# Kernel tuning notes

Measured on AMD Instinct MI355X. Metric: run time of the kernel, lower is better.

The kernel has to match this reference:

```python
import jax, jax.numpy as jnp
import numpy as np

H = 516      # LSTM hidden per direction
T = 512      # encoder source length
B = 64       # batch
NY = 20      # decoder target length
SEQ = 20     # seqLen == decoder input feature == n classes


def _u(key, shape, k):
    return jax.random.uniform(key, shape, jnp.float32, -k, k)


def setup_inputs() -> dict:
    key = jax.random.key(0)
    ks = jax.random.split(key, 26)
    kh = float(1.0 / np.sqrt(H))
    ka = float(1.0 / np.sqrt(2 * H * 2))
    inp = {}
    inp['x'] = jax.random.normal(ks[0], (T, B, 4), jnp.float32)
    inp['y'] = jax.random.normal(ks[1], (NY, B, SEQ), jnp.float32)
    inp['label'] = jax.random.randint(ks[2], (NY, B), 0, SEQ)
    inp['expand_W'] = _u(ks[3], (256, 4), 0.5)
    inp['expand_b'] = _u(ks[4], (256,), 0.5)
    # encoder biLSTM: 2 layers x 2 directions; PyTorch gate order i,f,g,o
    inp['eWi0'] = _u(ks[5], (2, 4 * H, 256), kh)
    inp['eWh0'] = _u(ks[6], (2, 4 * H, H), kh)
    inp['eb0'] = _u(ks[7], (2, 4 * H), kh)
    inp['eWi1'] = _u(ks[8], (2, 4 * H, 2 * H), kh)
    inp['eWh1'] = _u(ks[9], (2, 4 * H, H), kh)
    inp['eb1'] = _u(ks[10], (2, 4 * H), kh)
    # decoder biLSTM
    inp['dWi0'] = _u(ks[11], (2, 4 * H, SEQ), kh)
    inp['dWh0'] = _u(ks[12], (2, 4 * H, H), kh)
    inp['db0'] = _u(ks[13], (2, 4 * H), kh)
    inp['dWi1'] = _u(ks[14], (2, 4 * H, 2 * H), kh)
    inp['dWh1'] = _u(ks[15], (2, 4 * H, H), kh)
    inp['db1'] = _u(ks[16], (2, 4 * H), kh)
    # concat attention: Linear(2064, 1032) + v
    inp['attn_W'] = _u(ks[17], (2 * H, 4 * H), ka)
    inp['attn_b'] = _u(ks[18], (2 * H,), ka)
    inp['attn_v'] = _u(ks[19], (2 * H,), ka)
    inp['concat_W'] = _u(ks[20], (2 * H, 4 * H), ka)
    inp['concat_b'] = _u(ks[21], (2 * H,), ka)
    inp['out_W'] = _u(ks[22], (SEQ, 2 * H), float(1.0 / np.sqrt(2 * H)))
    inp['out_b'] = _u(ks[23], (SEQ,), float(1.0 / np.sqrt(2 * H)))
    return inp


def _cell(x, h, c, Wi, Wh, b):
    g = x @ Wi.T + h @ Wh.T + b
    i, f, gg, o = jnp.split(g, 4, axis=-1)
    c2 = jax.nn.sigmoid(f) * c + jax.nn.sigmoid(i) * jnp.tanh(gg)
    h2 = jax.nn.sigmoid(o) * jnp.tanh(c2)
    return h2, c2


def _run_dir(xs, h0, c0, Wi, Wh, b, reverse):
    def step(carry, xt):
        h, c = _cell(xt, carry[0], carry[1], Wi, Wh, b)
        return (h, c), h
    (hT, cT), ys = jax.lax.scan(step, (h0, c0), xs, reverse=reverse)
    return ys, hT, cT


def _bilstm(xs, Wi0, Wh0, b0, Wi1, Wh1, b1):
    z = jnp.zeros((xs.shape[1], H), xs.dtype)
    out = xs
    hs, cs = [], []
    for Wi, Wh, b in ((Wi0, Wh0, b0), (Wi1, Wh1, b1)):
        yf, hf, cf = _run_dir(out, z, z, Wi[0], Wh[0], b[0], False)
        yb, hb, cb = _run_dir(out, z, z, Wi[1], Wh[1], b[1], True)
        out = jnp.concatenate([yf, yb], -1)
        hs += [hf, hb]
        cs += [cf, cb]
    return out, jnp.stack(hs), jnp.stack(cs)


def reference(x, y, label, expand_W, expand_b, eWi0, eWh0, eb0, eWi1, eWh1, eb1,
              dWi0, dWh0, db0, dWi1, dWh1, db1, attn_W, attn_b, attn_v,
              concat_W, concat_b, out_W, out_b):
    xe = x @ expand_W.T + expand_b                       # [T,B,256]
    outenc, h0, c0 = _bilstm(xe, eWi0, eWh0, eb0, eWi1, eWh1, eb1)  # [T,B,1032],[4,B,H]
    lab = label.astype(jnp.int32)

    def dec_step(carry, inp):
        h, c, loss = carry
        yi, li = inp                                    # [B,SEQ], [B]
        # 1-step bidirectional 2-layer decoder LSTM (seq len 1 => fwd==bwd path)
        h0f, c0f = _cell(yi, h[0], c[0], dWi0[0], dWh0[0], db0[0])
        h0b, c0b = _cell(yi, h[1], c[1], dWi0[1], dWh0[1], db0[1])
        l0 = jnp.concatenate([h0f, h0b], -1)
        h1f, c1f = _cell(l0, h[2], c[2], dWi1[0], dWh1[0], db1[0])
        h1b, c1b = _cell(l0, h[3], c[3], dWi1[1], dWh1[1], db1[1])
        outdec = jnp.concatenate([h1f, h1b], -1)        # [B,1032]
        # concat attention over encoder outputs
        hid = jnp.broadcast_to(outdec[None], outenc.shape)
        energy = jnp.tanh(jnp.concatenate([hid, outenc], -1) @ attn_W.T + attn_b)
        score = jnp.einsum('h,tbh->tb', attn_v, energy)
        aw = jax.nn.softmax(score, axis=0)              # softmax over src_len
        context = jnp.einsum('tb,tbh->bh', aw, outenc)
        co = jnp.tanh(jnp.concatenate([outdec, context], -1) @ concat_W.T + concat_b)
        logits = co @ out_W.T + out_b                   # [B,SEQ]
        ls = jax.nn.log_softmax(logits, -1)
        ce = -jnp.take_along_axis(ls, li[:, None], 1).mean()
        h_new = jnp.stack([h0f, h0b, h1f, h1b])
        c_new = jnp.stack([c0f, c0b, c1f, c1b])
        return (h_new, c_new, loss + ce), None

    init = (h0, c0, jnp.float32(0.0))
    (_, _, loss), _ = jax.lax.scan(dec_step, init, (y, lab))
    return loss
```

## Files before the change

kernel.cpp:

```cpp
#include <hip/hip_runtime.h>
#include <hip/hip_bf16.h>
#include <cstdint>

typedef __attribute__((ext_vector_type(8))) short s8v;
typedef __attribute__((ext_vector_type(4))) float f4v;

#define DEV __device__ __forceinline__

constexpr int Hh  = 516;
constexpr int HP  = 544;
constexpr int FH  = 2064;
constexpr int NP  = 2176;
constexpr int TT  = 512;
constexpr int BB  = 64;
constexpr int LD2 = 1088;
constexpr int LDE = 1152;
constexpr int CS  = 528;
constexpr int XR  = 584;

DEV float bf2f(unsigned short u){ return __builtin_bit_cast(float, (unsigned)u<<16); }
DEV unsigned short f2bf(float f){
  unsigned u = __builtin_bit_cast(unsigned, f);
  u += 0x7fffu + ((u>>16)&1u);
  return (unsigned short)(u>>16);
}
DEV float sigf(float x){ return 1.f/(1.f+__expf(-x)); }
DEV float tanhfast(float x){ float e=__expf(2.f*x); return 1.f - 2.f/(e+1.f); }

DEV __attribute__((always_inline))
unsigned long long aload(const unsigned long long* p){
  return __hip_atomic_load(p, __ATOMIC_RELAXED, __HIP_MEMORY_SCOPE_AGENT);
}

DEV void cell_x1(f4v (&acc)[4],
                 const unsigned short* __restrict__ X1, int ld1,
                 const unsigned short* __restrict__ W1, int ldw1, int K1,
                 int j0)
{
  const int tid = threadIdx.x;
  const int w = tid>>6, lane = tid&63, p = lane&15, q = lane>>4;
  const unsigned short* wrow = W1 + (size_t)(w*HP + j0 + p)*ldw1 + q*8;
  for (int kk = 0; kk < (K1>>5); ++kk) {
    s8v bfr = *(const s8v*)(wrow + (size_t)kk*32);
    #pragma unroll
    for (int m = 0; m < 4; ++m) {
      s8v afr = *(const s8v*)(X1 + (size_t)(m*16+p)*ld1 + kk*32 + q*8);
      acc[m] = __builtin_amdgcn_mfma_f32_16x16x32_bf16(afr, bfr, acc[m], 0, 0, 0);
    }
  }
}

template<bool BYP>
DEV void cell_rest(f4v (&acc)[4],
                   const unsigned short* __restrict__ X2g,
                   const unsigned short* __restrict__ W2,
                   const float* __restrict__ bias,
                   float* __restrict__ cst,
                   unsigned* __restrict__ hout,
                   unsigned short* __restrict__ yout, int ldy, int ycol,
                   int j0)
{
  __shared__ __align__(16) unsigned short Xs[64*XR];
  __shared__ float gbuf[4][64][17];
  const int tid = threadIdx.x;
  const int w = tid>>6, lane = tid&63, p = lane&15, q = lane>>4;

  {
    int row = tid >> 2, c4 = (tid & 3) * 4;
    unsigned long long tmp[34];
    #pragma unroll
    for (int it = 0; it < 34; ++it) {
      const unsigned long long* s =
        (const unsigned long long*)(X2g + (size_t)row*HP + it*16 + c4);
      tmp[it] = BYP ? aload(s) : *s;
    }
    #pragma unroll
    for (int it = 0; it < 34; ++it)
      *(unsigned long long*)(Xs + row*XR + it*16 + c4) = tmp[it];
  }
  __syncthreads();

  {
    const unsigned short* wrow = W2 + (size_t)(w*HP + j0 + p)*HP + q*8;
    #pragma unroll
    for (int kk = 0; kk < HP/32; ++kk) {
      s8v bfr = *(const s8v*)(wrow + kk*32);
      #pragma unroll
      for (int m = 0; m < 4; ++m) {
        s8v afr = *(const s8v*)(Xs + (m*16+p)*XR + kk*32 + q*8);
        acc[m] = __builtin_amdgcn_mfma_f32_16x16x32_bf16(afr, bfr, acc[m], 0, 0, 0);
      }
    }
  }
  {
    int j = j0 + p;
    float bval = (j < Hh) ? bias[w*Hh + j] : 0.f;
    #pragma unroll
    for (int m = 0; m < 4; ++m)
      #pragma unroll
      for (int r = 0; r < 4; ++r)
        gbuf[w][m*16 + q*4 + r][p] = acc[m][r] + bval;
  }
  __syncthreads();
  {
    int b = tid & 63, j4 = tid >> 6;
    unsigned short hb[4];
    #pragma unroll
    for (int ii = 0; ii < 4; ++ii) {
      int jj = j4*4 + ii, jg = j0 + jj;
      float gi = gbuf[0][b][jj], gf = gbuf[1][b][jj];
      float gg = gbuf[2][b][jj], go = gbuf[3][b][jj];
      bool valid = jg < Hh;
      float c  = valid ? cst[(size_t)b*CS + jg] : 0.f;
      float c2 = sigf(gf)*c + sigf(gi)*tanhfast(gg);
      float h  = sigf(go)*tanhfast(c2);
      if (valid) cst[(size_t)b*CS + jg] = c2;
      hb[ii] = valid ? f2bf(h) : (unsigned short)0;
    }
    unsigned hu0 = (unsigned)hb[0] | ((unsigned)hb[1] << 16);
    unsigned hu1 = (unsigned)hb[2] | ((unsigned)hb[3] << 16);
    unsigned* hp = hout + (size_t)b*(HP/2) + (j0 + j4*4)/2;
    __hip_atomic_store(hp,   hu0, __ATOMIC_RELAXED, __HIP_MEMORY_SCOPE_AGENT);
    __hip_atomic_store(hp+1, hu1, __ATOMIC_RELAXED, __HIP_MEMORY_SCOPE_AGENT);
    unsigned long long yv = (unsigned long long)hu0 | ((unsigned long long)hu1 << 32);
    *(unsigned long long*)(yout + (size_t)b*ldy + ycol + j0 + j4*4) = yv;
  }
  __syncthreads();
}

__global__ void __launch_bounds__(256) enc_rnn(
  const unsigned short* __restrict__ Wi,
  int ldwi, int K1,
  const unsigned short* __restrict__ Xseq,
  int ld1,
  const unsigned short* __restrict__ Wh,
  const float* __restrict__ eb,
  unsigned short* __restrict__ yout,
  unsigned short* __restrict__ hbufs,
  float* __restrict__ cst,
  unsigned* flags)
{
  int d = blockIdx.x / 33, j0 = (blockIdx.x % 33) * 16;
  const unsigned short* W1 = Wi + (size_t)d*NP*ldwi;
  const unsigned short* W2 = Wh + (size_t)d*NP*HP;
  const float* bias = eb + (size_t)d*FH;
  float* cs = cst + (size_t)d*BB*CS;
  unsigned* flg = flags + (size_t)d*TT;
  for (int t = 0; t < TT; ++t) {
    int tf = d ? (TT-1-t) : t;
    const unsigned short* hin = hbufs + (size_t)((t&1)*2 + d)*BB*HP;
    unsigned* hout = (unsigned*)(hbufs + (size_t)(((t+1)&1)*2 + d)*BB*HP);
    f4v acc[4] = {};
    cell_x1(acc, Xseq + (size_t)tf*BB*ld1, ld1, W1, ldwi, K1, j0);
    if (t > 0 && threadIdx.x == 0) {
      while (__hip_atomic_load(flg + (t-1), __ATOMIC_RELAXED,
                               __HIP_MEMORY_SCOPE_AGENT) < 33u)
        __builtin_amdgcn_s_sleep(1);
    }
    __syncthreads();
    cell_rest<true>(acc, hin, W2, bias, cs, hout,
                    yout + (size_t)tf*BB*LD2, LD2, d*HP, j0);
    if (threadIdx.x == 0)
      __hip_atomic_fetch_add(flg + t, 1u, __ATOMIC_RELAXED, __HIP_MEMORY_SCOPE_AGENT);
  }
}

__global__ void __launch_bounds__(256) dec_cell(
  const unsigned short* __restrict__ X1, int ld1, int K1,
  const unsigned short* __restrict__ hin_base,
  unsigned short* __restrict__ hout_base,
  int loff,
  const unsigned short* __restrict__ Wi, int ldwi,
  const unsigned short* __restrict__ Whh,
  const float* __restrict__ dbias,
  float* __restrict__ cstates,
  unsigned short* __restrict__ yout, int ldy)
{
  int d = blockIdx.x / 33, j0 = (blockIdx.x % 33) * 16;
  f4v acc[4] = {};
  cell_x1(acc, X1, ld1, Wi + (size_t)d*NP*ldwi, ldwi, K1, j0);
  cell_rest<false>(acc,
    hin_base + (size_t)(loff+d)*BB*HP,
    Whh + (size_t)d*NP*HP,
    dbias + (size_t)d*FH,
    cstates + (size_t)(loff+d)*BB*CS,
    (unsigned*)(hout_base + (size_t)(loff+d)*BB*HP),
    yout, ldy, d*HP, j0);
}

__global__ void __launch_bounds__(256) gemm_bt(
  const unsigned short* __restrict__ A, int lda,
  const unsigned short* __restrict__ W, int ldw,
  unsigned short* __restrict__ C, int ldc, int K,
  const float* __restrict__ bias, int nbias)
{
  __shared__ __align__(16) unsigned short As[128*72];
  __shared__ __align__(16) unsigned short Ws[128*72];
  int tid = threadIdx.x, w = tid>>6, lane = tid&63, p = lane&15, q = lane>>4;
  int wm = w & 1, wn = w >> 1;
  size_t m0 = (size_t)blockIdx.x * 128;
  int n0 = blockIdx.y * 128;
  f4v acc[4][4] = {};
  for (int k0 = 0; k0 < K; k0 += 64) {
    __syncthreads();
    #pragma unroll
    for (int i = 0; i < 4; ++i) {
      int v = tid + i*256;
      int row = v >> 3, k8 = (v & 7) * 8;
      *(s8v*)(As + row*72 + k8) = *(const s8v*)(A + (m0+row)*lda + k0 + k8);
      *(s8v*)(Ws + row*72 + k8) = *(const s8v*)(W + (size_t)(n0+row)*ldw + k0 + k8);
    }
    __syncthreads();
    #pragma unroll
    for (int kk = 0; kk < 2; ++kk) {
      s8v af[4], bf[4];
      #pragma unroll
      for (int i = 0; i < 4; ++i) {
        af[i] = *(const s8v*)(As + (wm*64 + i*16 + p)*72 + kk*32 + q*8);
        bf[i] = *(const s8v*)(Ws + (wn*64 + i*16 + p)*72 + kk*32 + q*8);
      }
      #pragma unroll
      for (int mt = 0; mt < 4; ++mt)
        #pragma unroll
        for (int nt = 0; nt < 4; ++nt)
          acc[mt][nt] = __builtin_amdgcn_mfma_f32_16x16x32_bf16(af[mt], bf[nt], acc[mt][nt], 0,0,0);
    }
  }
  #pragma unroll
  for (int mt = 0; mt < 4; ++mt)
    #pragma unroll
    for (int nt = 0; nt < 4; ++nt)
      #pragma unroll
      for (int r = 0; r < 4; ++r) {
        size_t row = m0 + wm*64 + mt*16 + q*4 + r;
        int col = n0 + wn*64 + nt*16 + p;
        float v = acc[mt][nt][r];
        if (bias && col < nbias) v += bias[col];
        C[row*ldc + col] = f2bf(v);
      }
}

__global__ void __launch_bounds__(256) gemm64(
  const unsigned short* __restrict__ A, int lda,
  const unsigned short* __restrict__ W, int ldw, int K,
  const float* __restrict__ bias, int nbias, int mode,
  void* __restrict__ C, int ldc)
{
  int tid = threadIdx.x, w = tid>>6, lane = tid&63, p = lane&15, q = lane>>4;
  int n0 = blockIdx.x*64 + w*16;
  f4v acc[4] = {};
  const unsigned short* wrow = W + (size_t)(n0+p)*ldw + q*8;
  for (int kk = 0; kk < K/32; ++kk) {
    s8v bfr = *(const s8v*)(wrow + kk*32);
    #pragma unroll
    for (int m = 0; m < 4; ++m) {
      s8v afr = *(const s8v*)(A + (size_t)(m*16+p)*lda + kk*32 + q*8);
      acc[m] = __builtin_amdgcn_mfma_f32_16x16x32_bf16(afr, bfr, acc[m], 0,0,0);
    }
  }
  #pragma unroll
  for (int m = 0; m < 4; ++m)
    #pragma unroll
    for (int r = 0; r < 4; ++r) {
      int b = m*16 + q*4 + r, col = n0 + p;
      float v = acc[m][r];
      if (bias && col < nbias) v += bias[col];
      if (mode == 2) v = tanhfast(v);
      if (mode == 0) ((float*)C)[(size_t)b*ldc + col] = v;
      else ((unsigned short*)C)[(size_t)b*ldc + col] = f2bf(v);
    }
}

__global__ void __launch_bounds__(256) attn_score(
  const unsigned short* __restrict__ encp,
  const float* __restrict__ qv,
  const float* __restrict__ av,
  float* __restrict__ score)
{
  int t = blockIdx.x;
  int w = threadIdx.x>>6, lane = threadIdx.x&63;
  float vv[17];
  #pragma unroll
  for (int i = 0; i < 17; ++i) { int n = i*64+lane; vv[i] = (n < 1032) ? av[n] : 0.f; }
  const unsigned short* erow = encp + (size_t)t*BB*LDE;
  for (int bb = 0; bb < 16; ++bb) {
    int b = w*16 + bb;
    const unsigned short* e = erow + (size_t)b*LDE;
    const float* qb = qv + (size_t)b*LDE;
    float s = 0.f;
    #pragma unroll
    for (int i = 0; i < 17; ++i) {
      int n = i*64 + lane;
      s += vv[i] * tanhfast(bf2f(e[n]) + qb[n]);
    }
    #pragma unroll
    for (int off = 32; off; off >>= 1) s += __shfl_xor(s, off);
    if (lane == 0) score[(size_t)t*BB + b] = s;
  }
}

__global__ void __launch_bounds__(256) attn_ctx(
  const float* __restrict__ score,
  const unsigned short* __restrict__ outenc,
  unsigned short* __restrict__ Xc)
{
  __shared__ float aw[512];
  __shared__ float red[4];
  int tid = threadIdx.x, w = tid>>6, lane = tid&63;
  int b = blockIdx.x >> 1, half = blockIdx.x & 1;
  float s0 = score[(size_t)tid*BB + b];
  float s1 = score[(size_t)(tid+256)*BB + b];
  float m = fmaxf(s0, s1);
  #pragma unroll
  for (int off = 32; off; off >>= 1) m = fmaxf(m, __shfl_xor(m, off));
  if (lane == 0) red[w] = m;
  __syncthreads();
  m = fmaxf(fmaxf(red[0], red[1]), fmaxf(red[2], red[3]));
  __syncthreads();
  float e0 = __expf(s0 - m), e1 = __expf(s1 - m);
  aw[tid] = e0; aw[tid+256] = e1;
  float ss = e0 + e1;
  #pragma unroll
  for (int off = 32; off; off >>= 1) ss += __shfl_xor(ss, off);
  if (lane == 0) red[w] = ss;
  __syncthreads();
  float inv = 1.f / (red[0]+red[1]+red[2]+red[3]);
  float acc0 = 0.f, acc1 = 0.f, acc2 = 0.f;
  const unsigned short* base = outenc + (size_t)b*LD2 + half*HP;
  for (int t = 0; t < 512; ++t) {
    float a_ = aw[t];
    const unsigned short* orow = base + (size_t)t*BB*LD2;
    acc0 += a_ * bf2f(orow[tid]);
    acc1 += a_ * bf2f(orow[tid+256]);
    if (tid < 32) acc2 += a_ * bf2f(orow[tid+512]);
  }
  unsigned short* dst = Xc + (size_t)b*2176 + 1088 + half*HP;
  dst[tid]      = f2bf(acc0*inv);
  dst[tid+256]  = f2bf(acc1*inv);
  if (tid < 32) dst[tid+512] = f2bf(acc2*inv);
}

__global__ void ce_k(const float* __restrict__ logits,
                     const int* __restrict__ label,
                     float* __restrict__ out)
{
  int b = threadIdx.x;
  const float* lr = logits + (size_t)b*64;
  float m = -1e30f;
  for (int n = 0; n < 20; ++n) m = fmaxf(m, lr[n]);
  float s = 0.f;
  for (int n = 0; n < 20; ++n) s += __expf(lr[n] - m);
  int li = label[b];
  float ce = -(lr[li] - m - __logf(s));
  #pragma unroll
  for (int off = 32; off; off >>= 1) ce += __shfl_xor(ce, off);
  if (b == 0) atomicAdd(out, ce * (1.f/64.f));
}

__global__ void __launch_bounds__(256) expand_k(
  const float* __restrict__ x, const float* __restrict__ eW,
  const float* __restrict__ ebi, unsigned short* __restrict__ xe)
{
  int row = blockIdx.x, j = threadIdx.x;
  const float* xr = x + (size_t)row*4;
  float4 wv = ((const float4*)eW)[j];
  float v = ebi[j] + xr[0]*wv.x + xr[1]*wv.y + xr[2]*wv.z + xr[3]*wv.w;
  xe[(size_t)row*256 + j] = f2bf(v);
}

__global__ void __launch_bounds__(256) dec_init(
  const unsigned short* __restrict__ encH,
  const float* __restrict__ encC,
  unsigned short* __restrict__ decH,
  float* __restrict__ decC)
{
  int tid = blockIdx.x*256 + threadIdx.x;
  int nth = gridDim.x*256;
  for (int i = tid; i < 4*BB*HP; i += nth) {
    int k = i / (BB*HP), rem = i % (BB*HP);
    decH[i] = encH[((size_t)(k>>1)*4 + (k&1))*BB*HP + rem];
  }
  for (int i = tid; i < 4*BB*CS; i += nth) {
    int k = i / (BB*CS), rem = i % (BB*CS);
    decC[i] = encC[((size_t)(k>>1)*2 + (k&1))*BB*CS + rem];
  }
}

struct PackA {
  const float *eWi0,*eWh0,*eWi1,*eWh1,*dWi0,*dWh0,*dWi1,*dWh1,*aW,*cW,*oW,*y;
  unsigned short *pEWi0,*pEWh0,*pEWi1,*pEWh1,*pDWi0,*pDWh0,*pDWi1,*pDWh1,
                 *pAW1,*pAW2,*pCW,*pOW,*pY;
};

__global__ void __launch_bounds__(256) pack_k(PackA a){
  int job = blockIdx.y, row = blockIdx.x, tid = threadIdx.x;
  if (job < 16) {
    if (row >= NP) return;
    int d = job & 1, jt = job >> 1;
    int g = row / HP, jj = row % HP; bool vr = jj < Hh; int sr = g*Hh + jj;
    if (jt == 0) {
      unsigned short* dst = a.pEWi0 + ((size_t)d*NP + row)*256;
      const float* s = a.eWi0 + ((size_t)d*FH + sr)*256;
      for (int k = tid; k < 256; k += 256) dst[k] = vr ? f2bf(s[k]) : 0;
    } else if (jt == 1) {
      unsigned short* dst = a.pEWh0 + ((size_t)d*NP + row)*HP;
      const float* s = a.eWh0 + ((size_t)d*FH + sr)*Hh;
      for (int k = tid; k < HP; k += 256) dst[k] = (vr && k < Hh) ? f2bf(s[k]) : 0;
    } else if (jt == 2) {
      unsigned short* dst = a.pEWi1 + ((size_t)d*NP + row)*LD2;
      const float* s = a.eWi1 + ((size_t)d*FH + sr)*1032;
      for (int k = tid; k < LD2; k += 256) {
        int d2 = k/HP, j = k%HP;
        dst[k] = (vr && j < Hh) ? f2bf(s[d2*Hh + j]) : 0;
      }
    } else if (jt == 3) {
      unsigned short* dst = a.pEWh1 + ((size_t)d*NP + row)*HP;
      const float* s = a.eWh1 + ((size_t)d*FH + sr)*Hh;
      for (int k = tid; k < HP; k += 256) dst[k] = (vr && k < Hh) ? f2bf(s[k]) : 0;
    } else if (jt == 4) {
      unsigned short* dst = a.pDWi0 + ((size_t)d*NP + row)*64;
      const float* s = a.dWi0 + ((size_t)d*FH + sr)*20;
      for (int k = tid; k < 64; k += 256) dst[k] = (vr && k < 20) ? f2bf(s[k]) : 0;
    } else if (jt == 5) {
      unsigned short* dst = a.pDWh0 + ((size_t)d*NP + row)*HP;
      const float* s = a.dWh0 + ((size_t)d*FH + sr)*Hh;
      for (int k = tid; k < HP; k += 256) dst[k] = (vr && k < Hh) ? f2bf(s[k]) : 0;
    } else if (jt == 6) {
      unsigned short* dst = a.pDWi1 + ((size_t)d*NP + row)*LD2;
      const float* s = a.dWi1 + ((size_t)d*FH + sr)*1032;
      for (int k = tid; k < LD2; k += 256) {
        int d2 = k/HP, j = k%HP;
        dst[k] = (vr && j < Hh) ? f2bf(s[d2*Hh + j]) : 0;
      }
    } else {
      unsigned short* dst = a.pDWh1 + ((size_t)d*NP + row)*HP;
      const float* s = a.dWh1 + ((size_t)d*FH + sr)*Hh;
      for (int k = tid; k < HP; k += 256) dst[k] = (vr && k < Hh) ? f2bf(s[k]) : 0;
    }
  } else if (job == 16 || job == 17) {
    if (row >= LDE) return;
    bool vr = row < 1032;
    unsigned short* dst = (job == 16 ? a.pAW1 : a.pAW2) + (size_t)row*LD2;
    int off = (job == 16 ? 0 : 1032);
    for (int k = tid; k < LD2; k += 256) {
      int d2 = k/HP, j = k%HP;
      dst[k] = (vr && j < Hh) ? f2bf(a.aW[(size_t)row*FH + off + d2*Hh + j]) : 0;
    }
  } else if (job == 18) {
    if (row >= LDE) return;
    bool vr = row < 1032;
    unsigned short* dst = a.pCW + (size_t)row*2176;
    for (int k = tid; k < 2176; k += 256) {
      int half = k/LD2, r2 = k%LD2, d2 = r2/HP, j = r2%HP;
      dst[k] = (vr && j < Hh) ? f2bf(a.cW[(size_t)row*FH + half*1032 + d2*Hh + j]) : 0;
    }
  } else if (job == 19) {
    if (row >= 64) return;
    unsigned short* dst = a.pOW + (size_t)row*LD2;
    for (int k = tid; k < LD2; k += 256)
      dst[k] = (row < 20 && k < 1032) ? f2bf(a.oW[(size_t)row*1032 + k]) : 0;
  } else {
    if (row >= 1280) return;
    unsigned short* dst = a.pY + (size_t)row*64;
    for (int k = tid; k < 64; k += 256)
      dst[k] = (k < 20) ? f2bf(a.y[(size_t)row*20 + k]) : 0;
  }
}

extern "C" void kernel_launch(void* const* d_in, const int* in_sizes, int n_in,
                              void* d_out, int out_size, void* d_ws, size_t ws_size,
                              hipStream_t stream) {
  const float* x    = (const float*)d_in[0];
  const float* y    = (const float*)d_in[1];
  const int* label  = (const int*)d_in[2];
  const float* expW = (const float*)d_in[3];
  const float* expb = (const float*)d_in[4];
  const float* eWi0 = (const float*)d_in[5];
  const float* eWh0 = (const float*)d_in[6];
  const float* eb0  = (const float*)d_in[7];
  const float* eWi1 = (const float*)d_in[8];
  const float* eWh1 = (const float*)d_in[9];
  const float* eb1  = (const float*)d_in[10];
  const float* dWi0 = (const float*)d_in[11];
  const float* dWh0 = (const float*)d_in[12];
  const float* db0  = (const float*)d_in[13];
  const float* dWi1 = (const float*)d_in[14];
  const float* dWh1 = (const float*)d_in[15];
  const float* db1  = (const float*)d_in[16];
  const float* attW = (const float*)d_in[17];
  const float* attb = (const float*)d_in[18];
  const float* attv = (const float*)d_in[19];
  const float* cW   = (const float*)d_in[20];
  const float* cb   = (const float*)d_in[21];
  const float* oW   = (const float*)d_in[22];
  const float* ob   = (const float*)d_in[23];

  char* base = (char*)d_ws;
  size_t o = 0;
  auto alloc = [&](size_t bytes){ size_t r = o; o = (o + bytes + 255) & ~(size_t)255; return r; };

  size_t o_encH  = alloc((size_t)2*2*2*BB*HP*2);
  size_t o_decH  = alloc((size_t)2*4*BB*HP*2);
  size_t o_l0    = alloc((size_t)BB*LD2*2);
  size_t o_Xc    = alloc((size_t)BB*2176*2);
  size_t o_encC  = alloc((size_t)2*2*BB*CS*4);
  size_t o_decC  = alloc((size_t)4*BB*CS*4);
  size_t o_flags = alloc((size_t)2*2*TT*4);
  size_t ZB = o;
  size_t o_xe    = alloc((size_t)TT*BB*256*2);
  size_t o_big   = alloc((size_t)TT*BB*LDE*2);
  size_t o_oenc  = alloc((size_t)TT*BB*LD2*2);
  size_t o_pEWi0 = alloc((size_t)2*NP*256*2);
  size_t o_pEWh0 = alloc((size_t)2*NP*HP*2);
  size_t o_pEWi1 = alloc((size_t)2*NP*LD2*2);
  size_t o_pEWh1 = alloc((size_t)2*NP*HP*2);
  size_t o_pDWi0 = alloc((size_t)2*NP*64*2);
  size_t o_pDWh0 = alloc((size_t)2*NP*HP*2);
  size_t o_pDWi1 = alloc((size_t)2*NP*LD2*2);
  size_t o_pDWh1 = alloc((size_t)2*NP*HP*2);
  size_t o_pAW1  = alloc((size_t)LDE*LD2*2);
  size_t o_pAW2  = alloc((size_t)LDE*LD2*2);
  size_t o_pCW   = alloc((size_t)LDE*2176*2);
  size_t o_pOW   = alloc((size_t)64*LD2*2);
  size_t o_pY    = alloc((size_t)1280*64*2);
  size_t o_q     = alloc((size_t)BB*LDE*4);
  size_t o_score = alloc((size_t)TT*BB*4);
  size_t o_co    = alloc((size_t)BB*LD2*2);
  size_t o_log   = alloc((size_t)BB*64*4);
  (void)in_sizes; (void)n_in; (void)out_size;

  if (o > ws_size) return;

  unsigned short* encH = (unsigned short*)(base + o_encH);
  unsigned short* decH = (unsigned short*)(base + o_decH);
  unsigned short* l0   = (unsigned short*)(base + o_l0);
  unsigned short* Xc   = (unsigned short*)(base + o_Xc);
  float* encC = (float*)(base + o_encC);
  float* decC = (float*)(base + o_decC);
  unsigned* flags = (unsigned*)(base + o_flags);
  unsigned short* xe   = (unsigned short*)(base + o_xe);
  unsigned short* y0   = (unsigned short*)(base + o_big);
  unsigned short* encp = (unsigned short*)(base + o_big);
  unsigned short* oenc = (unsigned short*)(base + o_oenc);
  unsigned short* pEWi0 = (unsigned short*)(base + o_pEWi0);
  unsigned short* pEWh0 = (unsigned short*)(base + o_pEWh0);
  unsigned short* pEWi1 = (unsigned short*)(base + o_pEWi1);
  unsigned short* pEWh1 = (unsigned short*)(base + o_pEWh1);
  unsigned short* pDWi0 = (unsigned short*)(base + o_pDWi0);
  unsigned short* pDWh0 = (unsigned short*)(base + o_pDWh0);
  unsigned short* pDWi1 = (unsigned short*)(base + o_pDWi1);
  unsigned short* pDWh1 = (unsigned short*)(base + o_pDWh1);
  unsigned short* pAW1 = (unsigned short*)(base + o_pAW1);
  unsigned short* pAW2 = (unsigned short*)(base + o_pAW2);
  unsigned short* pCW  = (unsigned short*)(base + o_pCW);
  unsigned short* pOW  = (unsigned short*)(base + o_pOW);
  unsigned short* pY   = (unsigned short*)(base + o_pY);
  float* qbuf  = (float*)(base + o_q);
  float* score = (float*)(base + o_score);
  unsigned short* co = (unsigned short*)(base + o_co);
  float* logits = (float*)(base + o_log);

  hipMemsetAsync(d_ws, 0, ZB, stream);
  hipMemsetAsync(d_out, 0, sizeof(float), stream);

  PackA pa;
  pa.eWi0 = eWi0; pa.eWh0 = eWh0; pa.eWi1 = eWi1; pa.eWh1 = eWh1;
  pa.dWi0 = dWi0; pa.dWh0 = dWh0; pa.dWi1 = dWi1; pa.dWh1 = dWh1;
  pa.aW = attW; pa.cW = cW; pa.oW = oW; pa.y = y;
  pa.pEWi0 = pEWi0; pa.pEWh0 = pEWh0; pa.pEWi1 = pEWi1; pa.pEWh1 = pEWh1;
  pa.pDWi0 = pDWi0; pa.pDWh0 = pDWh0; pa.pDWi1 = pDWi1; pa.pDWh1 = pDWh1;
  pa.pAW1 = pAW1; pa.pAW2 = pAW2; pa.pCW = pCW; pa.pOW = pOW; pa.pY = pY;
  pack_k<<<dim3(NP, 21), 256, 0, stream>>>(pa);

  expand_k<<<TT*BB, 256, 0, stream>>>(x, expW, expb, xe);

  enc_rnn<<<66, 256, 0, stream>>>(pEWi0, 256, 256, xe, 256,
      pEWh0, eb0, y0, encH, encC, flags);
  enc_rnn<<<66, 256, 0, stream>>>(pEWi1, LD2, LD2, y0, LD2,
      pEWh1, eb1, oenc, encH + (size_t)2*2*BB*HP, encC + (size_t)2*BB*CS,
      flags + 2*TT);

  dec_init<<<64, 256, 0, stream>>>(encH, encC, decH, decC);

  gemm_bt<<<dim3(256, 9), 256, 0, stream>>>(
      oenc, LD2, pAW2, LD2, encp, LDE, LD2, attb, 1032);

  const size_t DHB = (size_t)4*BB*HP;
  for (int s = 0; s < 20; ++s) {
    int p = s & 1, p2 = p ^ 1;
    dec_cell<<<66, 256, 0, stream>>>(
      pY + (size_t)s*64*64, 64, 64, decH + (size_t)p*DHB, decH + (size_t)p2*DHB, 0,
      pDWi0, 64, pDWh0, db0, decC, l0, LD2);
    dec_cell<<<66, 256, 0, stream>>>(
      l0, LD2, LD2, decH + (size_t)p*DHB, decH + (size_t)p2*DHB, 2,
      pDWi1, LD2, pDWh1, db1, decC, Xc, 2176);
    gemm64<<<18, 256, 0, stream>>>(Xc, 2176, pAW1, LD2, LD2, nullptr, 0, 0, qbuf, LDE);
    attn_score<<<512, 256, 0, stream>>>(encp, qbuf, attv, score);
    attn_ctx<<<128, 256, 0, stream>>>(score, oenc, Xc);
    gemm64<<<17, 256, 0, stream>>>(Xc, 2176, pCW, 2176, 2176, cb, 1032, 2, co, LD2);
    gemm64<<<1, 256, 0, stream>>>(co, LD2, pOW, LD2, LD2, ob, 20, 0, logits, 64);
    ce_k<<<1, 64, 0, stream>>>(logits, label + (size_t)s*64, (float*)d_out);
  }
}
```

Before: 26.52 ms.

## Read recurrent hidden state from sequence output and use per-block ready flags

The encoder recurrence no longer keeps separate double-buffered hidden-state arrays. Each step reads the previous hidden state directly from the layer output sequence, written with atomic stores. The shared counter flag is replaced by per-block flag slots, which a full wavefront polls in parallel instead of one thread waiting on a fetch-add counter. The hidden-state staging load also switches from relaxed 64-bit atomic loads to plain 128-bit vector loads, which drops the duplicate stores and widens the loads on the serial critical path. The risk is memory-visibility ordering, since relaxed flag stores paired with non-atomic reads could let a block read stale data.

```diff
diff --git a/kernel.cpp b/kernel.cpp
--- a/kernel.cpp
+++ b/kernel.cpp
@@ -27,11 +27,6 @@
 DEV float sigf(float x){ return 1.f/(1.f+__expf(-x)); }
 DEV float tanhfast(float x){ float e=__expf(2.f*x); return 1.f - 2.f/(e+1.f); }
 
-DEV __attribute__((always_inline))
-unsigned long long aload(const unsigned long long* p){
-  return __hip_atomic_load(p, __ATOMIC_RELAXED, __HIP_MEMORY_SCOPE_AGENT);
-}
-
 DEV void cell_x1(f4v (&acc)[4],
                  const unsigned short* __restrict__ X1, int ld1,
                  const unsigned short* __restrict__ W1, int ldw1, int K1,
@@ -50,13 +45,13 @@
   }
 }
 
-template<bool BYP>
+template<bool AST>
 DEV void cell_rest(f4v (&acc)[4],
-                   const unsigned short* __restrict__ X2g,
+                   const unsigned short* __restrict__ X2g, int ldx2,
                    const unsigned short* __restrict__ W2,
                    const float* __restrict__ bias,
                    float* __restrict__ cst,
-                   unsigned* __restrict__ hout,
+                   unsigned short* __restrict__ hout,
                    unsigned short* __restrict__ yout, int ldy, int ycol,
                    int j0)
 {
@@ -66,17 +61,14 @@
   const int w = tid>>6, lane = tid&63, p = lane&15, q = lane>>4;
 
   {
-    int row = tid >> 2, c4 = (tid & 3) * 4;
-    unsigned long long tmp[34];
-    #pragma unroll
-    for (int it = 0; it < 34; ++it) {
-      const unsigned long long* s =
-        (const unsigned long long*)(X2g + (size_t)row*HP + it*16 + c4);
-      tmp[it] = BYP ? aload(s) : *s;
-    }
-    #pragma unroll
-    for (int it = 0; it < 34; ++it)
-      *(unsigned long long*)(Xs + row*XR + it*16 + c4) = tmp[it];
+    int r = tid >> 2, c = tid & 3;
+    const char* src = (const char*)X2g + (size_t)r*(ldx2*2) + c*16;
+    char* dst = (char*)Xs + (size_t)r*(XR*2) + c*16;
+    s8v tmp[17];
+    #pragma unroll
+    for (int k = 0; k < 17; ++k) tmp[k] = *(const s8v*)(src + (size_t)k*64);
+    #pragma unroll
+    for (int k = 0; k < 17; ++k) *(s8v*)(dst + k*64) = tmp[k];
   }
   __syncthreads();
 
@@ -119,11 +111,15 @@
     }
     unsigned hu0 = (unsigned)hb[0] | ((unsigned)hb[1] << 16);
     unsigned hu1 = (unsigned)hb[2] | ((unsigned)hb[3] << 16);
-    unsigned* hp = hout + (size_t)b*(HP/2) + (j0 + j4*4)/2;
-    __hip_atomic_store(hp,   hu0, __ATOMIC_RELAXED, __HIP_MEMORY_SCOPE_AGENT);
-    __hip_atomic_store(hp+1, hu1, __ATOMIC_RELAXED, __HIP_MEMORY_SCOPE_AGENT);
     unsigned long long yv = (unsigned long long)hu0 | ((unsigned long long)hu1 << 32);
-    *(unsigned long long*)(yout + (size_t)b*ldy + ycol + j0 + j4*4) = yv;
+    unsigned long long* yp =
+      (unsigned long long*)(yout + (size_t)b*ldy + ycol + j0 + j4*4);
+    if (AST)
+      __hip_atomic_store(yp, yv, __ATOMIC_RELAXED, __HIP_MEMORY_SCOPE_AGENT);
+    else
+      *yp = yv;
+    if (hout)
+      *(unsigned long long*)(hout + (size_t)b*HP + j0 + j4*4) = yv;
   }
   __syncthreads();
 }
@@ -136,32 +132,42 @@
   const unsigned short* __restrict__ Wh,
   const float* __restrict__ eb,
   unsigned short* __restrict__ yout,
-  unsigned short* __restrict__ hbufs,
+  const unsigned short* __restrict__ hz,
   float* __restrict__ cst,
-  unsigned* flags)
-{
-  int d = blockIdx.x / 33, j0 = (blockIdx.x % 33) * 16;
+  unsigned* __restrict__ flags)
+{
+  int d = blockIdx.x / 33, slot = blockIdx.x % 33, j0 = slot * 16;
   const unsigned short* W1 = Wi + (size_t)d*NP*ldwi;
   const unsigned short* W2 = Wh + (size_t)d*NP*HP;
   const float* bias = eb + (size_t)d*FH;
   float* cs = cst + (size_t)d*BB*CS;
-  unsigned* flg = flags + (size_t)d*TT;
+  unsigned* flg = flags + (size_t)d*TT*64;
   for (int t = 0; t < TT; ++t) {
     int tf = d ? (TT-1-t) : t;
-    const unsigned short* hin = hbufs + (size_t)((t&1)*2 + d)*BB*HP;
-    unsigned* hout = (unsigned*)(hbufs + (size_t)(((t+1)&1)*2 + d)*BB*HP);
     f4v acc[4] = {};
     cell_x1(acc, Xseq + (size_t)tf*BB*ld1, ld1, W1, ldwi, K1, j0);
-    if (t > 0 && threadIdx.x == 0) {
-      while (__hip_atomic_load(flg + (t-1), __ATOMIC_RELAXED,
-                               __HIP_MEMORY_SCOPE_AGENT) < 33u)
+    if (t > 0 && threadIdx.x < 64) {
+      const unsigned* f = flg + (size_t)(t-1)*64;
+      while (true) {
+        unsigned v = (threadIdx.x < 33)
+          ? __hip_atomic_load(f + threadIdx.x, __ATOMIC_RELAXED, __HIP_MEMORY_SCOPE_AGENT)
+          : 1u;
+        if (__all((int)(v != 0))) break;
         __builtin_amdgcn_s_sleep(1);
+      }
     }
     __syncthreads();
-    cell_rest<true>(acc, hin, W2, bias, cs, hout,
+    const unsigned short* X2g; int ldx2;
+    if (t == 0) { X2g = hz; ldx2 = HP; }
+    else {
+      int tp = d ? (TT - t) : (t - 1);
+      X2g = yout + (size_t)tp*BB*LD2 + d*HP; ldx2 = LD2;
+    }
+    cell_rest<true>(acc, X2g, ldx2, W2, bias, cs, nullptr,
                     yout + (size_t)tf*BB*LD2, LD2, d*HP, j0);
     if (threadIdx.x == 0)
-      __hip_atomic_fetch_add(flg + t, 1u, __ATOMIC_RELAXED, __HIP_MEMORY_SCOPE_AGENT);
+      __hip_atomic_store(flg + (size_t)t*64 + slot, 1u,
+                         __ATOMIC_RELAXED, __HIP_MEMORY_SCOPE_AGENT);
   }
 }
 
@@ -180,11 +186,11 @@
   f4v acc[4] = {};
   cell_x1(acc, X1, ld1, Wi + (size_t)d*NP*ldwi, ldwi, K1, j0);
   cell_rest<false>(acc,
-    hin_base + (size_t)(loff+d)*BB*HP,
+    hin_base + (size_t)(loff+d)*BB*HP, HP,
     Whh + (size_t)d*NP*HP,
     dbias + (size_t)d*FH,
     cstates + (size_t)(loff+d)*BB*CS,
-    (unsigned*)(hout_base + (size_t)(loff+d)*BB*HP),
+    hout_base + (size_t)(loff+d)*BB*HP,
     yout, ldy, d*HP, j0);
 }
 
@@ -369,7 +375,8 @@
 }
 
 __global__ void __launch_bounds__(256) dec_init(
-  const unsigned short* __restrict__ encH,
+  const unsigned short* __restrict__ y0,
+  const unsigned short* __restrict__ oenc,
   const float* __restrict__ encC,
   unsigned short* __restrict__ decH,
   float* __restrict__ decC)
@@ -378,7 +385,10 @@
   int nth = gridDim.x*256;
   for (int i = tid; i < 4*BB*HP; i += nth) {
     int k = i / (BB*HP), rem = i % (BB*HP);
-    decH[i] = encH[((size_t)(k>>1)*4 + (k&1))*BB*HP + rem];
+    int b = rem / HP, j = rem % HP;
+    const unsigned short* src = (k < 2) ? y0 : oenc;
+    int t = (k & 1) ? 0 : (TT-1);
+    decH[i] = src[(size_t)t*BB*LD2 + (size_t)b*LD2 + (k&1)*HP + j];
   }
   for (int i = tid; i < 4*BB*CS; i += nth) {
     int k = i / (BB*CS), rem = i % (BB*CS);
@@ -499,13 +509,13 @@
   size_t o = 0;
   auto alloc = [&](size_t bytes){ size_t r = o; o = (o + bytes + 255) & ~(size_t)255; return r; };
 
-  size_t o_encH  = alloc((size_t)2*2*2*BB*HP*2);
+  size_t o_hz    = alloc((size_t)BB*HP*2);
   size_t o_decH  = alloc((size_t)2*4*BB*HP*2);
   size_t o_l0    = alloc((size_t)BB*LD2*2);
   size_t o_Xc    = alloc((size_t)BB*2176*2);
   size_t o_encC  = alloc((size_t)2*2*BB*CS*4);
   size_t o_decC  = alloc((size_t)4*BB*CS*4);
-  size_t o_flags = alloc((size_t)2*2*TT*4);
+  size_t o_flags = alloc((size_t)2*2*TT*64*4);
   size_t ZB = o;
   size_t o_xe    = alloc((size_t)TT*BB*256*2);
   size_t o_big   = alloc((size_t)TT*BB*LDE*2);
@@ -531,7 +541,7 @@
 
   if (o > ws_size) return;
 
-  unsigned short* encH = (unsigned short*)(base + o_encH);
+  unsigned short* hz   = (unsigned short*)(base + o_hz);
   unsigned short* decH = (unsigned short*)(base + o_decH);
   unsigned short* l0   = (unsigned short*)(base + o_l0);
   unsigned short* Xc   = (unsigned short*)(base + o_Xc);
@@ -575,12 +585,11 @@
   expand_k<<<TT*BB, 256, 0, stream>>>(x, expW, expb, xe);
 
   enc_rnn<<<66, 256, 0, stream>>>(pEWi0, 256, 256, xe, 256,
-      pEWh0, eb0, y0, encH, encC, flags);
+      pEWh0, eb0, y0, hz, encC, flags);
   enc_rnn<<<66, 256, 0, stream>>>(pEWi1, LD2, LD2, y0, LD2,
-      pEWh1, eb1, oenc, encH + (size_t)2*2*BB*HP, encC + (size_t)2*BB*CS,
-      flags + 2*TT);
-
-  dec_init<<<64, 256, 0, stream>>>(encH, encC, decH, decC);
+      pEWh1, eb1, oenc, hz, encC + (size_t)2*BB*CS, flags + (size_t)2*TT*64);
+
+  dec_init<<<64, 256, 0, stream>>>(y0, oenc, encC, decH, decC);
 
   gemm_bt<<<dim3(256, 9), 256, 0, stream>>>(
       oenc, LD2, pAW2, LD2, encp, LDE, LD2, attb, 1032);
```

New measurement: 24.34 ms. 8.2% less time.
